# Kernel tuning notes

Measured on AMD Instinct MI355X. Metric: run time of the kernel, lower is better.

The kernel has to match this reference:

```python
import jax, jax.numpy as jnp
import numpy as np
import math

MSG_K = 256  # min(active_count, 256); with uniform(0,1) activations active_count >> 256
N_HEADS = 4
LN_EPS = 1e-5


def _mha(x, wi, bi, wo, bo):
    # torch nn.MultiheadAttention self-attention, batch_first=True
    B, K, D = x.shape
    H = N_HEADS
    hd = D // H
    qkv = x @ wi.T + bi                      # [B,K,3D]
    q, k, v = jnp.split(qkv, 3, axis=-1)
    def split_heads(t):
        return t.reshape(B, K, H, hd).transpose(0, 2, 1, 3)  # [B,H,K,hd]
    q, k, v = split_heads(q), split_heads(k), split_heads(v)
    scores = jnp.einsum('bhqd,bhkd->bhqk', q, k) * (1.0 / math.sqrt(hd))
    attn = jax.nn.softmax(scores, axis=-1)
    o = jnp.einsum('bhqk,bhkd->bhqd', attn, v)
    o = o.transpose(0, 2, 1, 3).reshape(B, K, D)
    return o @ wo.T + bo


def _layernorm(x, g, b):
    mu = jnp.mean(x, axis=-1, keepdims=True)
    var = jnp.mean((x - mu) ** 2, axis=-1, keepdims=True)
    return (x - mu) * jax.lax.rsqrt(var + LN_EPS) * g + b


def setup_inputs() -> dict:
    key = jax.random.key(0)
    ks = jax.random.split(key, 12)
    B, N, D = 32, 4096, 256
    s = 0.02
    return {
        'activation': jax.random.uniform(ks[0], (B, N), dtype=jnp.float32),
        'hidden_state': jax.random.normal(ks[1], (B, N, D), dtype=jnp.float32),
        'in_proj_w': jax.random.normal(ks[2], (3 * D, D), dtype=jnp.float32) * s,
        'in_proj_b': jnp.zeros((3 * D,), jnp.float32),
        'out_proj_w': jax.random.normal(ks[3], (D, D), dtype=jnp.float32) * s,
        'out_proj_b': jnp.zeros((D,), jnp.float32),
        'su_w1': jax.random.normal(ks[4], (D, 2 * D), dtype=jnp.float32) * s,
        'su_b1': jnp.zeros((D,), jnp.float32),
        'su_w2': jax.random.normal(ks[5], (D, D), dtype=jnp.float32) * s,
        'su_b2': jnp.zeros((D,), jnp.float32),
        'au_w1': jax.random.normal(ks[6], (D, 2 * D), dtype=jnp.float32) * s,
        'au_b1': jnp.zeros((D,), jnp.float32),
        'au_w2': jax.random.normal(ks[7], (1, D), dtype=jnp.float32) * s,
        'au_b2': jnp.zeros((1,), jnp.float32),
        'ln_g': jnp.ones((D,), jnp.float32),
        'ln_b': jnp.zeros((D,), jnp.float32),
        'sparsity_k': 256,
    }


def reference(activation, hidden_state, in_proj_w, in_proj_b, out_proj_w, out_proj_b,
              su_w1, su_b1, su_w2, su_b2, au_w1, au_b1, au_w2, au_b2, ln_g, ln_b,
              sparsity_k):
    B, N, D = hidden_state.shape
    b_idx = jnp.arange(B)[:, None]

    # ---- compute_messages: top-k gather -> sparse MHA -> scatter back ----
    topk_vals, topk_idx = jax.lax.top_k(activation, MSG_K)        # [B,K]
    active_states = jnp.take_along_axis(hidden_state, topk_idx[..., None], axis=1)  # [B,K,D]
    msg_sparse = _mha(active_states, in_proj_w, in_proj_b, out_proj_w, out_proj_b)
    msg_sparse = msg_sparse * topk_vals[..., None]
    messages = jnp.zeros((B, N, D), hidden_state.dtype).at[b_idx, topk_idx].set(msg_sparse)

    # ---- update_states: MLP on [old, messages] + LayerNorm ----
    combined = jnp.concatenate([hidden_state, messages], axis=-1)  # [B,N,2D]
    h = jax.nn.gelu(combined @ su_w1.T + su_b1, approximate=False)
    new_hidden = _layernorm(h @ su_w2.T + su_b2, ln_g, ln_b)

    # ---- update_activations ----
    comb2 = jnp.concatenate([hidden_state, new_hidden], axis=-1)
    h2 = jax.nn.gelu(comb2 @ au_w1.T + au_b1, approximate=False)
    delta = jax.nn.sigmoid((h2 @ au_w2.T + au_b2).squeeze(-1))     # [B,N]
    new_activation = jnp.clip(0.7 * activation + 0.3 * delta, 0.0, 1.0)

    # ---- maintain_sparsity: keep top sparsity_k, zero the rest ----
    k = min(int(sparsity_k), N)
    tv, ti = jax.lax.top_k(new_activation, k)                      # [B,k]
    sparse_act = jnp.zeros_like(new_activation).at[b_idx, ti].set(tv)
    kept_hidden = jnp.take_along_axis(new_hidden, ti[..., None], axis=1)
    sparse_hidden = jnp.zeros_like(new_hidden).at[b_idx, ti].set(kept_hidden)
    return sparse_act, sparse_hidden
```

## Files before the change

### kernel.cpp

```cpp
#include <hip/hip_runtime.h>


constexpr int KC = 32;
constexpr int CMAX = 2304;
constexpr float BAND_EPS = 0.01f;
constexpr int MAXBAND = 512;

typedef short bf16x8 __attribute__((ext_vector_type(8)));
typedef float f32x4 __attribute__((ext_vector_type(4)));

__device__ __forceinline__ float gelu_f(float x) {
    return 0.5f * x * (1.0f + erff(x * 0.70710678118654752440f));
}
__device__ __forceinline__ unsigned short f2bf(float f) {
    unsigned u = __float_as_uint(f);
    return (unsigned short)((u + 0x7fffu + ((u >> 16) & 1u)) >> 16);
}
__device__ __forceinline__ float bf2f(unsigned short h) {
    return __uint_as_float(((unsigned)h) << 16);
}

__global__ void __launch_bounds__(256) fill0_k(float4* p, long n4) {
    long i = (long)blockIdx.x * 256 + threadIdx.x;
    long stride = (long)gridDim.x * 256;
    float4 z = make_float4(0.f, 0.f, 0.f, 0.f);
    for (; i < n4; i += stride) p[i] = z;
}

__global__ void __launch_bounds__(256) topk1_k(const float* __restrict__ act,
        float* __restrict__ svals, int* __restrict__ sidx, int* __restrict__ cnt)
{
    __shared__ int cs[4];
    __shared__ int sTop, sRest;
    int b = blockIdx.x, tid = threadIdx.x;
    int wid = tid >> 6, lane = tid & 63;
    unsigned v[16];
    #pragma unroll
    for (int s = 0; s < 16; ++s)
        v[s] = __float_as_uint(act[b * 4096 + s * 256 + tid]);

    auto reduce4 = [&](int c) -> int {
        #pragma unroll
        for (int off = 32; off >= 1; off >>= 1) c += __shfl_xor(c, off);
        if (lane == 0) cs[wid] = c;
        __syncthreads();
        int tot = cs[0] + cs[1] + cs[2] + cs[3];
        __syncthreads();
        return tot;
    };
    auto countGE = [&](unsigned thr) -> int {
        int c = 0;
        #pragma unroll
        for (int s = 0; s < 16; ++s) c += (v[s] >= thr) ? 1 : 0;
        return reduce4(c);
    };
    auto countEqLt = [&](unsigned vs, int icut) -> int {
        int c = 0;
        #pragma unroll
        for (int s = 0; s < 16; ++s)
            c += (v[s] == vs && (s * 256 + tid) < icut) ? 1 : 0;
        return reduce4(c);
    };

    unsigned vstar = 0;
    for (int bit = 31; bit >= 0; --bit) {
        unsigned cand = vstar | (1u << bit);
        if (countGE(cand) >= 256) vstar = cand;
    }
    int cgt = countGE(vstar + 1);
    int needed = 256 - cgt;
    int icut = 4096;
    if (countEqLt(vstar, 4096) > needed) {
        int lo = 0, hi = 4096;
        for (int it = 0; it < 12; ++it) {
            int mid = (lo + hi) >> 1;
            if (countEqLt(vstar, mid) <= needed) lo = mid; else hi = mid;
        }
        icut = lo;
    }
    if (tid == 0) { sTop = 0; sRest = 0; }
    __syncthreads();
    float th = __uint_as_float(vstar) - 0.4288f;
    #pragma unroll
    for (int s = 0; s < 16; ++s) {
        int i = s * 256 + tid;
        unsigned vb = v[s];
        float f = __uint_as_float(vb);
        bool top = (vb > vstar) || (vb == vstar && i < icut);
        if (top) {
            int slot = atomicAdd(&sTop, 1);
            sidx[b * 4096 + slot] = i;
            svals[b * 4096 + slot] = f;
        } else if (f >= th) {
            int slot = 256 + atomicAdd(&sRest, 1);
            if (slot < CMAX) {
                sidx[b * 4096 + slot] = i;
                svals[b * 4096 + slot] = f;
            }
        }
    }
    __syncthreads();
    if (tid == 0) cnt[b] = min(256 + sRest, CMAX);
}

__global__ void __launch_bounds__(256) topk2_k(const float* __restrict__ newact,
        const int* __restrict__ sidx, const int* __restrict__ cnt,
        float* __restrict__ selv, int* __restrict__ selo, int* __restrict__ selp)
{
    __shared__ int cs[4];
    __shared__ int sSel;
    int b = blockIdx.x, tid = threadIdx.x;
    int wid = tid >> 6, lane = tid & 63;
    int C = min(cnt[b], CMAX);
    unsigned v[9];
    int org[9];
    #pragma unroll
    for (int s = 0; s < 9; ++s) {
        int p = s * 256 + tid;
        bool ok = (p < C && p < CMAX);
        v[s] = ok ? __float_as_uint(newact[(long)b * CMAX + p]) : 0u;
        org[s] = ok ? sidx[b * 4096 + p] : 0x7FFFFFFF;
    }
    auto reduce4 = [&](int c) -> int {
        #pragma unroll
        for (int off = 32; off >= 1; off >>= 1) c += __shfl_xor(c, off);
        if (lane == 0) cs[wid] = c;
        __syncthreads();
        int tot = cs[0] + cs[1] + cs[2] + cs[3];
        __syncthreads();
        return tot;
    };
    auto countGE = [&](unsigned thr) -> int {
        int c = 0;
        #pragma unroll
        for (int s = 0; s < 9; ++s) c += (v[s] >= thr) ? 1 : 0;
        return reduce4(c);
    };
    auto countEqLt = [&](unsigned vs, int icut) -> int {
        int c = 0;
        #pragma unroll
        for (int s = 0; s < 9; ++s) c += (v[s] == vs && org[s] < icut) ? 1 : 0;
        return reduce4(c);
    };

    unsigned vstar = 0;
    for (int bit = 31; bit >= 0; --bit) {
        unsigned cand = vstar | (1u << bit);
        if (countGE(cand) >= 256) vstar = cand;
    }
    int cgt = countGE(vstar + 1);
    int needed = 256 - cgt;
    int icut = 4096;
    if (countEqLt(vstar, 4096) > needed) {
        int lo = 0, hi = 4096;
        for (int it = 0; it < 12; ++it) {
            int mid = (lo + hi) >> 1;
            if (countEqLt(vstar, mid) <= needed) lo = mid; else hi = mid;
        }
        icut = lo;
    }
    if (tid == 0) sSel = 0;
    __syncthreads();
    #pragma unroll
    for (int s = 0; s < 9; ++s) {
        unsigned vb = v[s];
        bool sel = (vb > vstar) || (vb == vstar && org[s] < icut);
        if (sel) {
            int slot = atomicAdd(&sSel, 1);
            selv[b * 256 + slot] = __uint_as_float(vb);
            selo[b * 256 + slot] = org[s];
            selp[b * 256 + slot] = s * 256 + tid;
        }
    }
}

template<int TM, int TN, int RM, int RN, bool BT, bool GATHER, int EPI>
__global__ void __launch_bounds__(256) gemm_k(
    const float* __restrict__ A, int lda, long sA1, long sA2, int divA,
    const float* __restrict__ B, int ldb, long sB1, long sB2, int divB,
    float* __restrict__ C, int ldc, long sC1, long sC2, int divC,
    int K, const float* __restrict__ bias, const float* __restrict__ rowscale,
    long rsStride, const int* __restrict__ gmap, long gmapStride, float cscale)
{
    constexpr int TX = TN / RN, TY = TM / RM;
    static_assert(TX * TY == 256, "block must be 256 threads");
    __shared__ float As[KC][TM + 4];
    __shared__ float Bs[KC][TN + 4];
    int z = blockIdx.z;
    const float* Ab = A + (long)(z / divA) * sA1 + (long)(z % divA) * sA2;
    const float* Bb = B + (long)(z / divB) * sB1 + (long)(z % divB) * sB2;
    float* Cb = C + (long)(z / divC) * sC1 + (long)(z % divC) * sC2;
    int m0 = blockIdx.y * TM, n0 = blockIdx.x * TN;
    int tid = threadIdx.x;
    int tx = tid % TX, ty = tid / TX;
    float acc[RM][RN];
    #pragma unroll
    for (int i = 0; i < RM; ++i)
        #pragma unroll
        for (int j = 0; j < RN; ++j) acc[i][j] = 0.f;

    for (int k0 = 0; k0 < K; k0 += KC) {
        __syncthreads();
        #pragma unroll
        for (int u = 0; u < (TM * KC) / 1024; ++u) {
            int idx = tid + u * 256;
            int m = idx / (KC / 4), k4 = idx % (KC / 4);
            int row = m0 + m;
            long grow = GATHER ? (long)gmap[(long)z * gmapStride + row] : (long)row;
            float4 v = *(const float4*)(Ab + grow * lda + k0 + k4 * 4);
            As[k4 * 4 + 0][m] = v.x; As[k4 * 4 + 1][m] = v.y;
            As[k4 * 4 + 2][m] = v.z; As[k4 * 4 + 3][m] = v.w;
        }
        if (BT) {
            #pragma unroll
            for (int u = 0; u < (TN * KC) / 1024; ++u) {
                int idx = tid + u * 256;
                int n = idx / (KC / 4), k4 = idx % (KC / 4);
                float4 v = *(const float4*)(Bb + (long)(n0 + n) * ldb + k0 + k4 * 4);
                Bs[k4 * 4 + 0][n] = v.x; Bs[k4 * 4 + 1][n] = v.y;
                Bs[k4 * 4 + 2][n] = v.z; Bs[k4 * 4 + 3][n] = v.w;
            }
        } else {
            #pragma unroll
            for (int u = 0; u < (TN * KC) / 1024; ++u) {
                int idx = tid + u * 256;
                int k = idx / (TN / 4), n4 = idx % (TN / 4);
                float4 v = *(const float4*)(Bb + (long)(k0 + k) * ldb + n0 + n4 * 4);
                *(float4*)&Bs[k][n4 * 4] = v;
            }
        }
        __syncthreads();
        #pragma unroll
        for (int k = 0; k < KC; ++k) {
            float av[RM], bv[RN];
            #pragma unroll
            for (int i = 0; i < RM; i += 4) {
                float4 t = *(const float4*)&As[k][ty * RM + i];
                av[i] = t.x; av[i + 1] = t.y; av[i + 2] = t.z; av[i + 3] = t.w;
            }
            #pragma unroll
            for (int j = 0; j < RN; j += 4) {
                float4 t = *(const float4*)&Bs[k][tx * RN + j];
                bv[j] = t.x; bv[j + 1] = t.y; bv[j + 2] = t.z; bv[j + 3] = t.w;
            }
            #pragma unroll
            for (int i = 0; i < RM; ++i)
                #pragma unroll
                for (int j = 0; j < RN; ++j)
                    acc[i][j] = fmaf(av[i], bv[j], acc[i][j]);
        }
    }
    #pragma unroll
    for (int i = 0; i < RM; ++i) {
        int gm = m0 + ty * RM + i;
        float rs = 1.f;
        if (EPI == 2) rs = rowscale[(long)z * rsStride + gm];
        #pragma unroll
        for (int j = 0; j < RN; j += 4) {
            int gn = n0 + tx * RN + j;
            float4 v = make_float4(acc[i][j], acc[i][j + 1], acc[i][j + 2], acc[i][j + 3]);
            if (EPI == 1 || EPI == 2) {
                float4 bb = *(const float4*)(bias + gn);
                v.x += bb.x; v.y += bb.y; v.z += bb.z; v.w += bb.w;
            }
            if (EPI == 2) { v.x *= rs; v.y *= rs; v.z *= rs; v.w *= rs; }
            if (EPI == 3) { v.x *= cscale; v.y *= cscale; v.z *= cscale; v.w *= cscale; }
            *(float4*)(Cb + (long)gm * ldc + gn) = v;
        }
    }
}

__global__ void __launch_bounds__(256) softmax_k(float* __restrict__ S) {
    int row = blockIdx.x * 4 + (threadIdx.x >> 6);
    int lane = threadIdx.x & 63;
    float4* r = (float4*)(S + (long)row * 256);
    float4 v = r[lane];
    float m = fmaxf(fmaxf(v.x, v.y), fmaxf(v.z, v.w));
    for (int off = 32; off >= 1; off >>= 1) m = fmaxf(m, __shfl_xor(m, off));
    v.x = expf(v.x - m); v.y = expf(v.y - m); v.z = expf(v.z - m); v.w = expf(v.w - m);
    float s = v.x + v.y + v.z + v.w;
    for (int off = 32; off >= 1; off >>= 1) s += __shfl_xor(s, off);
    float inv = 1.f / s;
    v.x *= inv; v.y *= inv; v.z *= inv; v.w *= inv;
    r[lane] = v;
}

__global__ void __launch_bounds__(256) convw_k(
        const float* __restrict__ s1, const float* __restrict__ s2,
        const float* __restrict__ a1,
        unsigned short* __restrict__ o1, unsigned short* __restrict__ o2,
        unsigned short* __restrict__ o3)
{
    int i = blockIdx.x * 256 + threadIdx.x;
    o1[i] = f2bf(s1[i]);
    o3[i] = f2bf(a1[i]);
    if (i < 65536) o2[i] = f2bf(s2[i]);
}

__global__ void __launch_bounds__(256) transT_k(const float* __restrict__ src,
        int ld, int koff, float* __restrict__ dst)
{
    __shared__ float t[32][33];
    int k0 = blockIdx.x * 32, n0 = blockIdx.y * 32;
    int tx = threadIdx.x & 31, ty = threadIdx.x >> 5;
    #pragma unroll
    for (int yy = 0; yy < 4; ++yy) {
        int nl = ty * 4 + yy;
        t[nl][tx] = src[(long)(n0 + nl) * ld + koff + k0 + tx];
    }
    __syncthreads();
    #pragma unroll
    for (int yy = 0; yy < 4; ++yy) {
        int kl = ty * 4 + yy;
        dst[(long)(k0 + kl) * 256 + n0 + tx] = t[tx][kl];
    }
}

__global__ void __launch_bounds__(256) gatherX_k(const float* __restrict__ hid,
        const int* __restrict__ sidx, const int* __restrict__ cnt,
        unsigned short* __restrict__ Xb)
{
    int b = blockIdx.y;
    int C = min(cnt[b], CMAX);
    int p = blockIdx.x * 4 + (threadIdx.x >> 6);
    int lane = threadIdx.x & 63;
    unsigned short* dst = Xb + ((long)b * CMAX + p) * 256 + lane * 4;
    if (p < C) {
        int row = sidx[b * 4096 + p];
        float4 v = *(const float4*)(hid + ((long)b * 4096 + row) * 256 + lane * 4);
        ushort4 o; o.x = f2bf(v.x); o.y = f2bf(v.y); o.z = f2bf(v.z); o.w = f2bf(v.w);
        *(ushort4*)dst = o;
    } else {
        ushort4 z; z.x = 0; z.y = 0; z.z = 0; z.w = 0;
        *(ushort4*)dst = z;
    }
}

template<int STAGE>
__global__ void __launch_bounds__(256, 2) mlp_mfma_k(
    const unsigned short* __restrict__ A0,
    const unsigned short* __restrict__ A1,
    const unsigned short* __restrict__ W, int ldw,
    const float* __restrict__ bias,
    const float* __restrict__ msgc,
    const float* __restrict__ lng, const float* __restrict__ lnb,
    const float* __restrict__ w2v, const float* __restrict__ b2s,
    const float* __restrict__ svals,
    const int* __restrict__ cnt,
    unsigned short* __restrict__ outb,
    float* __restrict__ nac)
{
    int b = blockIdx.y;
    int C = min(cnt[b], CMAX);
    int m0 = blockIdx.x * 64;
    if (m0 >= C) return;
    int tid = threadIdx.x;
    int wid = tid >> 6;
    int lane = tid & 63;
    int l15 = lane & 15;
    int q = lane >> 4;
    int n0w = wid * 64;

    f32x4 acc[4][4];
    #pragma unroll
    for (int mt = 0; mt < 4; ++mt)
        #pragma unroll
        for (int nt = 0; nt < 4; ++nt) {
            f32x4 z = {0.f, 0.f, 0.f, 0.f};
            acc[mt][nt] = z;
        }

    const unsigned short* Ab = A0 + ((long)b * CMAX + m0) * 256;
    const unsigned short* A1b = (STAGE == 3) ? (A1 + ((long)b * CMAX + m0) * 256) : nullptr;
    int aoff[4];
    #pragma unroll
    for (int mt = 0; mt < 4; ++mt) aoff[mt] = (mt * 16 + l15) * 256;
    const unsigned short* wr[4];
    #pragma unroll
    for (int nt = 0; nt < 4; ++nt) wr[nt] = W + (long)(n0w + nt * 16 + l15) * ldw;

    constexpr int KSTEPS = (STAGE == 3) ? 16 : 8;
    #pragma unroll 4
    for (int ks = 0; ks < KSTEPS; ++ks) {
        const unsigned short* As = (STAGE == 3 && ks >= 8) ? A1b : Ab;
        int ko = (STAGE == 3 && ks >= 8) ? (ks - 8) * 32 : ks * 32;
        int kw = ks * 32;
        bf16x8 af[4], bfr[4];
        #pragma unroll
        for (int mt = 0; mt < 4; ++mt)
            af[mt] = *(const bf16x8*)(As + aoff[mt] + ko + q * 8);
        #pragma unroll
        for (int nt = 0; nt < 4; ++nt)
            bfr[nt] = *(const bf16x8*)(wr[nt] + kw + q * 8);
        #pragma unroll
        for (int mt = 0; mt < 4; ++mt)
            #pragma unroll
            for (int nt = 0; nt < 4; ++nt)
                acc[mt][nt] = __builtin_amdgcn_mfma_f32_16x16x32_bf16(
                    af[mt], bfr[nt], acc[mt][nt], 0, 0, 0);
    }

    if constexpr (STAGE == 1) {
        float bb[4];
        #pragma unroll
        for (int nt = 0; nt < 4; ++nt) bb[nt] = bias[n0w + nt * 16 + l15];
        #pragma unroll
        for (int mt = 0; mt < 4; ++mt) {
            #pragma unroll
            for (int reg = 0; reg < 4; ++reg) {
                int p = m0 + mt * 16 + q * 4 + reg;
                long orow = ((long)b * CMAX + p) * 256;
                const float* mrow = msgc + ((long)b * 256 + p) * 256;
                bool hasm = (p < 256);
                #pragma unroll
                for (int nt = 0; nt < 4; ++nt) {
                    int gc = n0w + nt * 16 + l15;
                    float v = acc[mt][nt][reg] + bb[nt];
                    if (hasm) v += mrow[gc];
                    outb[orow + gc] = f2bf(gelu_f(v));
                }
            }
        }
    }

    if constexpr (STAGE == 2) {
        __shared__ float rsum[4][64];
        __shared__ float rsq[4][64];
        __shared__ float rmu[64], rrs[64];
        float bb[4], gg[4], eb[4];
        #pragma unroll
        for (int nt = 0; nt < 4; ++nt) {
            int gc = n0w + nt * 16 + l15;
            bb[nt] = bias[gc]; gg[nt] = lng[gc]; eb[nt] = lnb[gc];
        }
        #pragma unroll
        for (int mt = 0; mt < 4; ++mt)
            #pragma unroll
            for (int nt = 0; nt < 4; ++nt)
                #pragma unroll
                for (int reg = 0; reg < 4; ++reg)
                    acc[mt][nt][reg] += bb[nt];
        #pragma unroll
        for (int mt = 0; mt < 4; ++mt) {
            #pragma unroll
            for (int reg = 0; reg < 4; ++reg) {
                float s = 0.f, s2 = 0.f;
                #pragma unroll
                for (int nt = 0; nt < 4; ++nt) {
                    float v = acc[mt][nt][reg];
                    s += v; s2 += v * v;
                }
                #pragma unroll
                for (int off = 1; off <= 8; off <<= 1) {
                    s += __shfl_xor(s, off);
                    s2 += __shfl_xor(s2, off);
                }
                if (l15 == 0) {
                    int row = mt * 16 + q * 4 + reg;
                    rsum[wid][row] = s; rsq[wid][row] = s2;
                }
            }
        }
        __syncthreads();
        if (tid < 64) {
            float s = rsum[0][tid] + rsum[1][tid] + rsum[2][tid] + rsum[3][tid];
            float s2 = rsq[0][tid] + rsq[1][tid] + rsq[2][tid] + rsq[3][tid];
            float mu = s * (1.f / 256.f);
            float var = s2 * (1.f / 256.f) - mu * mu;
            rmu[tid] = mu;
            rrs[tid] = rsqrtf(var + 1e-5f);
        }
        __syncthreads();
        #pragma unroll
        for (int mt = 0; mt < 4; ++mt) {
            #pragma unroll
            for (int reg = 0; reg < 4; ++reg) {
                int row = mt * 16 + q * 4 + reg;
                int p = m0 + row;
                float mu = rmu[row], rs = rrs[row];
                long orow = ((long)b * CMAX + p) * 256;
                #pragma unroll
                for (int nt = 0; nt < 4; ++nt) {
                    int gc = n0w + nt * 16 + l15;
                    outb[orow + gc] = f2bf((acc[mt][nt][reg] - mu) * rs * gg[nt] + eb[nt]);
                }
            }
        }
    }

    if constexpr (STAGE == 3) {
        __shared__ float rsum[4][64];
        float bb[4], ww[4];
        #pragma unroll
        for (int nt = 0; nt < 4; ++nt) {
            int gc = n0w + nt * 16 + l15;
            bb[nt] = bias[gc]; ww[nt] = w2v[gc];
        }
        #pragma unroll
        for (int mt = 0; mt < 4; ++mt) {
            #pragma unroll
            for (int reg = 0; reg < 4; ++reg) {
                float s = 0.f;
                #pragma unroll
                for (int nt = 0; nt < 4; ++nt)
                    s += gelu_f(acc[mt][nt][reg] + bb[nt]) * ww[nt];
                #pragma unroll
                for (int off = 1; off <= 8; off <<= 1) s += __shfl_xor(s, off);
                if (l15 == 0) rsum[wid][mt * 16 + q * 4 + reg] = s;
            }
        }
        __syncthreads();
        if (tid < 64) {
            int p = m0 + tid;
            if (p < C) {
                float z = rsum[0][tid] + rsum[1][tid] + rsum[2][tid] + rsum[3][tid] + b2s[0];
                float delta = 1.f / (1.f + expf(-z));
                float na = 0.7f * svals[b * 4096 + p] + 0.3f * delta;
                nac[(long)b * CMAX + p] = fminf(fmaxf(na, 0.f), 1.f);
            }
        }
    }
}

__global__ void __launch_bounds__(256) selectT_k(const float* __restrict__ nac,
        const int* __restrict__ cnt, float* __restrict__ T)
{
    __shared__ float v[CMAX];
    __shared__ int cs[256];
    __shared__ float bounds[2];
    int b = blockIdx.x, tid = threadIdx.x;
    int C = min(cnt[b], CMAX);
    for (int i = tid; i < CMAX; i += 256)
        v[i] = (i < C) ? nac[(long)b * CMAX + i] : -1.f;
    if (tid == 0) { bounds[0] = 0.f; bounds[1] = 1.0f; }
    __syncthreads();
    for (int it = 0; it < 30; ++it) {
        float mid = 0.5f * (bounds[0] + bounds[1]);
        int c = 0;
        for (int i = tid; i < CMAX; i += 256) c += (v[i] >= mid) ? 1 : 0;
        cs[tid] = c; __syncthreads();
        for (int s = 128; s; s >>= 1) {
            if (tid < s) cs[tid] += cs[tid + s];
            __syncthreads();
        }
        if (tid == 0) { if (cs[0] >= 256) bounds[0] = mid; else bounds[1] = mid; }
        __syncthreads();
    }
    if (tid == 0) T[b] = bounds[0];
}

__global__ void __launch_bounds__(256) bandlist_k(const float* __restrict__ nac,
        const int* __restrict__ cnt, const float* __restrict__ Tarr,
        int* __restrict__ bandlist, int* __restrict__ bandcnt)
{
    int b = blockIdx.y;
    int C = min(cnt[b], CMAX);
    int p = blockIdx.x * 256 + threadIdx.x;
    if (p < C && fabsf(nac[(long)b * CMAX + p] - Tarr[b]) < BAND_EPS) {
        int slot = atomicAdd(&bandcnt[b], 1);
        if (slot < MAXBAND) bandlist[b * MAXBAND + slot] = p;
    }
}

__global__ void __launch_bounds__(256) bandfix_k(
    const float* __restrict__ hid, const int* __restrict__ sidx,
    const float* __restrict__ msgc,
    const float* __restrict__ w1T, const float* __restrict__ su_b1,
    const float* __restrict__ w2T, const float* __restrict__ su_b2,
    const float* __restrict__ ln_g, const float* __restrict__ ln_b,
    const float* __restrict__ auT, const float* __restrict__ au_b1,
    const float* __restrict__ au_w2, const float* __restrict__ au_b2,
    const float* __restrict__ svals,
    const int* __restrict__ bandlist, const int* __restrict__ bandcnt,
    float* __restrict__ nac, unsigned short* __restrict__ NHb)
{
    int b = blockIdx.y;
    int M = min(bandcnt[b], MAXBAND);
    int base = blockIdx.x * 8;
    if (base >= M) return;
    int nact = min(M - base, 8);
    int tid = threadIdx.x;
    int wid = tid >> 6, lane = tid & 63;
    __shared__ float xr[8][256];
    __shared__ float hy[8][256];
    __shared__ float nh[8][256];
    __shared__ float muS[8], rsS[8];
    __shared__ int ppS[8];
    if (tid < 8)
        ppS[tid] = (tid < nact) ? bandlist[b * MAXBAND + base + tid] : -1;
    __syncthreads();
    #pragma unroll
    for (int r = 0; r < 8; ++r) {
        int pp = ppS[r];
        xr[r][tid] = (pp >= 0) ? hid[((long)b * 4096 + sidx[b * 4096 + pp]) * 256 + tid] : 0.f;
    }
    __syncthreads();
    int n = tid;
    float acc[8];
    #pragma unroll
    for (int r = 0; r < 8; ++r) acc[r] = 0.f;
    for (int k = 0; k < 256; k += 4) {
        float w0 = w1T[(k + 0) * 256 + n];
        float w1 = w1T[(k + 1) * 256 + n];
        float w2 = w1T[(k + 2) * 256 + n];
        float w3 = w1T[(k + 3) * 256 + n];
        #pragma unroll
        for (int r = 0; r < 8; ++r) {
            float4 xv = *(const float4*)&xr[r][k];
            acc[r] = fmaf(w0, xv.x, acc[r]);
            acc[r] = fmaf(w1, xv.y, acc[r]);
            acc[r] = fmaf(w2, xv.z, acc[r]);
            acc[r] = fmaf(w3, xv.w, acc[r]);
        }
    }
    float b1v = su_b1[n];
    #pragma unroll
    for (int r = 0; r < 8; ++r) {
        int pp = ppS[r];
        float s = acc[r] + b1v;
        if (pp >= 0 && pp < 256) s += msgc[((long)b * 256 + pp) * 256 + n];
        acc[r] = gelu_f(s);
    }
    __syncthreads();
    #pragma unroll
    for (int r = 0; r < 8; ++r) hy[r][n] = acc[r];
    __syncthreads();
    #pragma unroll
    for (int r = 0; r < 8; ++r) acc[r] = 0.f;
    for (int k = 0; k < 256; k += 4) {
        float w0 = w2T[(k + 0) * 256 + n];
        float w1 = w2T[(k + 1) * 256 + n];
        float w2 = w2T[(k + 2) * 256 + n];
        float w3 = w2T[(k + 3) * 256 + n];
        #pragma unroll
        for (int r = 0; r < 8; ++r) {
            float4 hv = *(const float4*)&hy[r][k];
            acc[r] = fmaf(w0, hv.x, acc[r]);
            acc[r] = fmaf(w1, hv.y, acc[r]);
            acc[r] = fmaf(w2, hv.z, acc[r]);
            acc[r] = fmaf(w3, hv.w, acc[r]);
        }
    }
    __syncthreads();
    float b2v = su_b2[n];
    #pragma unroll
    for (int r = 0; r < 8; ++r) hy[r][n] = acc[r] + b2v;
    __syncthreads();
    #pragma unroll
    for (int rr = 0; rr < 2; ++rr) {
        int r = wid + rr * 4;
        float4 yv = *(const float4*)&hy[r][lane * 4];
        float s = yv.x + yv.y + yv.z + yv.w;
        float s2 = yv.x * yv.x + yv.y * yv.y + yv.z * yv.z + yv.w * yv.w;
        #pragma unroll
        for (int off = 32; off >= 1; off >>= 1) {
            s += __shfl_xor(s, off);
            s2 += __shfl_xor(s2, off);
        }
        if (lane == 0) {
            float mu = s * (1.f / 256.f);
            float var = s2 * (1.f / 256.f) - mu * mu;
            muS[r] = mu; rsS[r] = rsqrtf(var + 1e-5f);
        }
    }
    __syncthreads();
    float gv = ln_g[n], ev = ln_b[n];
    #pragma unroll
    for (int r = 0; r < 8; ++r) {
        float o = (hy[r][n] - muS[r]) * rsS[r] * gv + ev;
        nh[r][n] = o;
        if (ppS[r] >= 0) NHb[((long)b * CMAX + ppS[r]) * 256 + n] = f2bf(o);
    }
    __syncthreads();
    #pragma unroll
    for (int r = 0; r < 8; ++r) acc[r] = 0.f;
    for (int k = 0; k < 256; k += 4) {
        float w0 = auT[(k + 0) * 256 + n];
        float w1 = auT[(k + 1) * 256 + n];
        float w2 = auT[(k + 2) * 256 + n];
        float w3 = auT[(k + 3) * 256 + n];
        #pragma unroll
        for (int r = 0; r < 8; ++r) {
            float4 xv = *(const float4*)&xr[r][k];
            acc[r] = fmaf(w0, xv.x, acc[r]);
            acc[r] = fmaf(w1, xv.y, acc[r]);
            acc[r] = fmaf(w2, xv.z, acc[r]);
            acc[r] = fmaf(w3, xv.w, acc[r]);
        }
    }
    for (int k = 0; k < 256; k += 4) {
        float w0 = auT[(256 + k + 0) * 256 + n];
        float w1 = auT[(256 + k + 1) * 256 + n];
        float w2 = auT[(256 + k + 2) * 256 + n];
        float w3 = auT[(256 + k + 3) * 256 + n];
        #pragma unroll
        for (int r = 0; r < 8; ++r) {
            float4 hv = *(const float4*)&nh[r][k];
            acc[r] = fmaf(w0, hv.x, acc[r]);
            acc[r] = fmaf(w1, hv.y, acc[r]);
            acc[r] = fmaf(w2, hv.z, acc[r]);
            acc[r] = fmaf(w3, hv.w, acc[r]);
        }
    }
    float ab = au_b1[n], wv2 = au_w2[n];
    __syncthreads();
    #pragma unroll
    for (int r = 0; r < 8; ++r) hy[r][n] = gelu_f(acc[r] + ab) * wv2;
    __syncthreads();
    #pragma unroll
    for (int rr = 0; rr < 2; ++rr) {
        int r = wid + rr * 4;
        float4 gvv = *(const float4*)&hy[r][lane * 4];
        float s = gvv.x + gvv.y + gvv.z + gvv.w;
        #pragma unroll
        for (int off = 32; off >= 1; off >>= 1) s += __shfl_xor(s, off);
        if (lane == 0 && ppS[r] >= 0) {
            float z = s + au_b2[0];
            float delta = 1.f / (1.f + expf(-z));
            float na = 0.7f * svals[b * 4096 + ppS[r]] + 0.3f * delta;
            nac[(long)b * CMAX + ppS[r]] = fminf(fmaxf(na, 0.f), 1.f);
        }
    }
}

__global__ void __launch_bounds__(64) scatter_k(const float* __restrict__ selv,
        const int* __restrict__ selo, const int* __restrict__ selp,
        const unsigned short* __restrict__ NHb, float* __restrict__ out)
{
    int b = blockIdx.x >> 8, j = blockIdx.x & 255, t = threadIdx.x;
    int orig = selo[b * 256 + j];
    int p = selp[b * 256 + j];
    if (t == 0) out[b * 4096 + orig] = selv[b * 256 + j];
    const ushort4* src = (const ushort4*)(NHb + ((long)b * CMAX + p) * 256);
    ushort4 s = src[t];
    float4 o = make_float4(bf2f(s.x), bf2f(s.y), bf2f(s.z), bf2f(s.w));
    *(float4*)(out + 131072 + ((long)(b * 4096 + orig)) * 256 + t * 4) = o;
}

extern "C" void kernel_launch(void* const* d_in, const int* in_sizes, int n_in,
                              void* d_out, int out_size, void* d_ws, size_t ws_size,
                              hipStream_t stream)
{
    const float* act   = (const float*)d_in[0];
    const float* hid   = (const float*)d_in[1];
    const float* wi    = (const float*)d_in[2];
    const float* bi    = (const float*)d_in[3];
    const float* wo    = (const float*)d_in[4];
    const float* bo    = (const float*)d_in[5];
    const float* su_w1 = (const float*)d_in[6];
    const float* su_b1 = (const float*)d_in[7];
    const float* su_w2 = (const float*)d_in[8];
    const float* su_b2 = (const float*)d_in[9];
    const float* au_w1 = (const float*)d_in[10];
    const float* au_b1 = (const float*)d_in[11];
    const float* au_w2 = (const float*)d_in[12];
    const float* au_b2 = (const float*)d_in[13];
    const float* ln_g  = (const float*)d_in[14];
    const float* ln_b  = (const float*)d_in[15];
    float* out = (float*)d_out;

    char* ws = (char*)d_ws;
    size_t off = 0;
    auto alloc = [&](size_t bytes) {
        size_t o = off; off += (bytes + 255) & ~(size_t)255; return o;
    };
    float* svals = (float*)(ws + alloc((size_t)32 * 4096 * 4));
    int*   sidx  = (int*)  (ws + alloc((size_t)32 * 4096 * 4));
    int*   cnt   = (int*)  (ws + alloc(256));
    float* qkv   = (float*)(ws + alloc((size_t)32 * 256 * 768 * 4));
    float* Sb    = (float*)(ws + alloc((size_t)32 * 4 * 256 * 256 * 4));
    float* Ob    = (float*)(ws + alloc((size_t)32 * 256 * 256 * 4));
    float* MSG   = (float*)(ws + alloc((size_t)32 * 256 * 256 * 4));
    float* MSGC  = (float*)(ws + alloc((size_t)32 * 256 * 256 * 4));
    float* selv  = (float*)(ws + alloc((size_t)32 * 256 * 4));
    int*   selo  = (int*)  (ws + alloc((size_t)32 * 256 * 4));
    int*   selp  = (int*)  (ws + alloc((size_t)32 * 256 * 4));
    unsigned short* swb1 = (unsigned short*)(ws + alloc((size_t)256 * 512 * 2));
    unsigned short* swb2 = (unsigned short*)(ws + alloc((size_t)256 * 256 * 2));
    unsigned short* awb1 = (unsigned short*)(ws + alloc((size_t)256 * 512 * 2));
    float* w1T = (float*)(ws + alloc((size_t)256 * 256 * 4));
    float* w2T = (float*)(ws + alloc((size_t)256 * 256 * 4));
    float* auT = (float*)(ws + alloc((size_t)512 * 256 * 4));
    unsigned short* Xb   = (unsigned short*)(ws + alloc((size_t)32 * CMAX * 256 * 2));
    unsigned short* H1b  = (unsigned short*)(ws + alloc((size_t)32 * CMAX * 256 * 2));
    unsigned short* NHb  = (unsigned short*)(ws + alloc((size_t)32 * CMAX * 256 * 2));
    float* nac = (float*)(ws + alloc((size_t)32 * CMAX * 4));
    float* Tb  = (float*)(ws + alloc(128));
    int* bandl = (int*)(ws + alloc((size_t)32 * MAXBAND * 4));
    int* bandc = (int*)(ws + alloc(128));

    hipMemsetAsync(bandc, 0, 32 * sizeof(int), stream);
    fill0_k<<<2048, 256, 0, stream>>>((float4*)out, (long)out_size / 4);
    topk1_k<<<32, 256, 0, stream>>>(act, svals, sidx, cnt);
    convw_k<<<512, 256, 0, stream>>>(su_w1, su_w2, au_w1, swb1, swb2, awb1);
    transT_k<<<dim3(8, 8), 256, 0, stream>>>(su_w1, 512, 0, w1T);
    transT_k<<<dim3(8, 8), 256, 0, stream>>>(su_w2, 256, 0, w2T);
    transT_k<<<dim3(16, 8), 256, 0, stream>>>(au_w1, 512, 0, auT);
    gatherX_k<<<dim3(CMAX / 4, 32), 256, 0, stream>>>(hid, sidx, cnt, Xb);
    gemm_k<64, 256, 8, 8, true, true, 1><<<dim3(3, 4, 32), 256, 0, stream>>>(
        hid, 256, (long)4096 * 256, 0, 1,
        wi, 256, 0, 0, 1,
        qkv, 768, (long)256 * 768, 0, 1,
        256, bi, nullptr, 0, sidx, 4096, 0.f);
    gemm_k<64, 256, 8, 8, true, false, 3><<<dim3(1, 4, 128), 256, 0, stream>>>(
        qkv, 768, 196608, 64, 4,
        qkv + 256, 768, 196608, 64, 4,
        Sb, 256, 65536, 0, 1,
        64, nullptr, nullptr, 0, nullptr, 0, 0.125f);
    softmax_k<<<8192, 256, 0, stream>>>(Sb);
    gemm_k<64, 64, 4, 4, false, false, 0><<<dim3(1, 4, 128), 256, 0, stream>>>(
        Sb, 256, 65536, 0, 1,
        qkv + 512, 768, 196608, 64, 4,
        Ob, 256, 65536, 64, 4,
        256, nullptr, nullptr, 0, nullptr, 0, 0.f);
    gemm_k<64, 256, 8, 8, true, false, 2><<<dim3(1, 4, 32), 256, 0, stream>>>(
        Ob, 256, 65536, 0, 1,
        wo, 256, 0, 0, 1,
        MSG, 256, 65536, 0, 1,
        256, bo, svals, 4096, nullptr, 0, 0.f);
    gemm_k<64, 256, 8, 8, true, false, 0><<<dim3(1, 4, 32), 256, 0, stream>>>(
        MSG, 256, 65536, 0, 1,
        su_w1 + 256, 512, 0, 0, 1,
        MSGC, 256, 65536, 0, 1,
        256, nullptr, nullptr, 0, nullptr, 0, 0.f);
    dim3 mgrid(CMAX / 64, 32);
    mlp_mfma_k<1><<<mgrid, 256, 0, stream>>>(Xb, nullptr, swb1, 512, su_b1, MSGC,
        nullptr, nullptr, nullptr, nullptr, nullptr, cnt, H1b, nullptr);
    mlp_mfma_k<2><<<mgrid, 256, 0, stream>>>(H1b, nullptr, swb2, 256, su_b2, nullptr,
        ln_g, ln_b, nullptr, nullptr, nullptr, cnt, NHb, nullptr);
    mlp_mfma_k<3><<<mgrid, 256, 0, stream>>>(Xb, NHb, awb1, 512, au_b1, nullptr,
        nullptr, nullptr, au_w2, au_b2, svals, cnt, nullptr, nac);
    selectT_k<<<32, 256, 0, stream>>>(nac, cnt, Tb);
    bandlist_k<<<dim3(CMAX / 256, 32), 256, 0, stream>>>(nac, cnt, Tb, bandl, bandc);
    bandfix_k<<<dim3(MAXBAND / 8, 32), 256, 0, stream>>>(hid, sidx, MSGC,
        w1T, su_b1, w2T, su_b2, ln_g, ln_b, auT, au_b1, au_w2, au_b2,
        svals, bandl, bandc, nac, NHb);
    topk2_k<<<32, 256, 0, stream>>>(nac, sidx, cnt, selv, selo, selp);
    scatter_k<<<8192, 64, 0, stream>>>(selv, selo, selp, NHb, out);
}
```

Before: 831.6 us.

## Pack fp32 weights as float4 for bandfix, fuse prep kernels, narrow refinement band

Merges the bf16 weight conversion and three transpose kernels into one prep kernel that writes the fp32 weights in a k-interleaved float4 layout. bandfix_k can then load a float4 per step instead of four scalars, and it now handles 4 rows per block instead of 8, giving more blocks. The exact-recompute band around the top-k threshold shrinks from 0.01 to 0.004, and the threshold bisection drops from 30 to 20 iterations. Together these cut launch count and the fp32 fix-up work. A narrower band and a coarser threshold could miss borderline candidates whose bf16 scores were wrong.

```diff
diff --git a/kernel.cpp b/kernel.cpp
--- a/kernel.cpp
+++ b/kernel.cpp
@@ -3,7 +3,7 @@
 
 constexpr int KC = 32;
 constexpr int CMAX = 2304;
-constexpr float BAND_EPS = 0.01f;
+constexpr float BAND_EPS = 0.004f;
 constexpr int MAXBAND = 512;
 
 typedef short bf16x8 __attribute__((ext_vector_type(8)));
@@ -285,34 +285,38 @@
     r[lane] = v;
 }
 
-__global__ void __launch_bounds__(256) convw_k(
+__global__ void __launch_bounds__(256) prep_k(
         const float* __restrict__ s1, const float* __restrict__ s2,
         const float* __restrict__ a1,
         unsigned short* __restrict__ o1, unsigned short* __restrict__ o2,
-        unsigned short* __restrict__ o3)
-{
-    int i = blockIdx.x * 256 + threadIdx.x;
-    o1[i] = f2bf(s1[i]);
-    o3[i] = f2bf(a1[i]);
-    if (i < 65536) o2[i] = f2bf(s2[i]);
-}
-
-__global__ void __launch_bounds__(256) transT_k(const float* __restrict__ src,
-        int ld, int koff, float* __restrict__ dst)
-{
+        unsigned short* __restrict__ o3,
+        float* __restrict__ w1P, float* __restrict__ w2P, float* __restrict__ auP)
+{
+    int blk = blockIdx.x, tid = threadIdx.x;
+    if (blk < 512) {
+        int i = blk * 256 + tid;
+        o1[i] = f2bf(s1[i]);
+        o3[i] = f2bf(a1[i]);
+        if (i < 65536) o2[i] = f2bf(s2[i]);
+        return;
+    }
+    const float* src; float* dst; int ld, ktiles, rel;
+    if (blk < 576) { rel = blk - 512; src = s1; ld = 512; dst = w1P; ktiles = 8; }
+    else if (blk < 640) { rel = blk - 576; src = s2; ld = 256; dst = w2P; ktiles = 8; }
+    else { rel = blk - 640; src = a1; ld = 512; dst = auP; ktiles = 16; }
+    int k0 = (rel % ktiles) * 32, n0 = (rel / ktiles) * 32;
     __shared__ float t[32][33];
-    int k0 = blockIdx.x * 32, n0 = blockIdx.y * 32;
-    int tx = threadIdx.x & 31, ty = threadIdx.x >> 5;
+    int tx = tid & 31, ty = tid >> 5;
     #pragma unroll
     for (int yy = 0; yy < 4; ++yy) {
         int nl = ty * 4 + yy;
-        t[nl][tx] = src[(long)(n0 + nl) * ld + koff + k0 + tx];
+        t[nl][tx] = src[(long)(n0 + nl) * ld + k0 + tx];
     }
     __syncthreads();
     #pragma unroll
     for (int yy = 0; yy < 4; ++yy) {
-        int kl = ty * 4 + yy;
-        dst[(long)(k0 + kl) * 256 + n0 + tx] = t[tx][kl];
+        int k = k0 + ty * 4 + yy;
+        dst[(long)(k >> 2) * 1024 + (n0 + tx) * 4 + (k & 3)] = t[tx][ty * 4 + yy];
     }
 }
 
@@ -534,7 +538,7 @@
         v[i] = (i < C) ? nac[(long)b * CMAX + i] : -1.f;
     if (tid == 0) { bounds[0] = 0.f; bounds[1] = 1.0f; }
     __syncthreads();
-    for (int it = 0; it < 30; ++it) {
+    for (int it = 0; it < 20; ++it) {
         float mid = 0.5f * (bounds[0] + bounds[1]);
         int c = 0;
         for (int i = tid; i < CMAX; i += 256) c += (v[i] >= mid) ? 1 : 0;
@@ -565,10 +569,10 @@
 __global__ void __launch_bounds__(256) bandfix_k(
     const float* __restrict__ hid, const int* __restrict__ sidx,
     const float* __restrict__ msgc,
-    const float* __restrict__ w1T, const float* __restrict__ su_b1,
-    const float* __restrict__ w2T, const float* __restrict__ su_b2,
+    const float* __restrict__ w1Pf, const float* __restrict__ su_b1,
+    const float* __restrict__ w2Pf, const float* __restrict__ su_b2,
     const float* __restrict__ ln_g, const float* __restrict__ ln_b,
-    const float* __restrict__ auT, const float* __restrict__ au_b1,
+    const float* __restrict__ auPf, const float* __restrict__ au_b1,
     const float* __restrict__ au_w2, const float* __restrict__ au_b2,
     const float* __restrict__ svals,
     const int* __restrict__ bandlist, const int* __restrict__ bandcnt,
@@ -576,46 +580,46 @@
 {
     int b = blockIdx.y;
     int M = min(bandcnt[b], MAXBAND);
-    int base = blockIdx.x * 8;
+    int base = blockIdx.x * 4;
     if (base >= M) return;
-    int nact = min(M - base, 8);
+    int nact = min(M - base, 4);
     int tid = threadIdx.x;
     int wid = tid >> 6, lane = tid & 63;
-    __shared__ float xr[8][256];
-    __shared__ float hy[8][256];
-    __shared__ float nh[8][256];
-    __shared__ float muS[8], rsS[8];
-    __shared__ int ppS[8];
-    if (tid < 8)
+    const float4* w1P = (const float4*)w1Pf;
+    const float4* w2P = (const float4*)w2Pf;
+    const float4* auP = (const float4*)auPf;
+    __shared__ float xr[4][256];
+    __shared__ float hy[4][256];
+    __shared__ float nh[4][256];
+    __shared__ float muS[4], rsS[4];
+    __shared__ int ppS[4];
+    if (tid < 4)
         ppS[tid] = (tid < nact) ? bandlist[b * MAXBAND + base + tid] : -1;
     __syncthreads();
     #pragma unroll
-    for (int r = 0; r < 8; ++r) {
+    for (int r = 0; r < 4; ++r) {
         int pp = ppS[r];
         xr[r][tid] = (pp >= 0) ? hid[((long)b * 4096 + sidx[b * 4096 + pp]) * 256 + tid] : 0.f;
     }
     __syncthreads();
     int n = tid;
-    float acc[8];
-    #pragma unroll
-    for (int r = 0; r < 8; ++r) acc[r] = 0.f;
-    for (int k = 0; k < 256; k += 4) {
-        float w0 = w1T[(k + 0) * 256 + n];
-        float w1 = w1T[(k + 1) * 256 + n];
-        float w2 = w1T[(k + 2) * 256 + n];
-        float w3 = w1T[(k + 3) * 256 + n];
-        #pragma unroll
-        for (int r = 0; r < 8; ++r) {
-            float4 xv = *(const float4*)&xr[r][k];
-            acc[r] = fmaf(w0, xv.x, acc[r]);
-            acc[r] = fmaf(w1, xv.y, acc[r]);
-            acc[r] = fmaf(w2, xv.z, acc[r]);
-            acc[r] = fmaf(w3, xv.w, acc[r]);
+    float acc[4];
+    #pragma unroll
+    for (int r = 0; r < 4; ++r) acc[r] = 0.f;
+    for (int k4 = 0; k4 < 64; ++k4) {
+        float4 w = w1P[k4 * 256 + n];
+        #pragma unroll
+        for (int r = 0; r < 4; ++r) {
+            float4 xv = *(const float4*)&xr[r][k4 * 4];
+            acc[r] = fmaf(w.x, xv.x, acc[r]);
+            acc[r] = fmaf(w.y, xv.y, acc[r]);
+            acc[r] = fmaf(w.z, xv.z, acc[r]);
+            acc[r] = fmaf(w.w, xv.w, acc[r]);
         }
     }
     float b1v = su_b1[n];
     #pragma unroll
-    for (int r = 0; r < 8; ++r) {
+    for (int r = 0; r < 4; ++r) {
         int pp = ppS[r];
         float s = acc[r] + b1v;
         if (pp >= 0 && pp < 256) s += msgc[((long)b * 256 + pp) * 256 + n];
@@ -623,32 +627,28 @@
     }
     __syncthreads();
     #pragma unroll
-    for (int r = 0; r < 8; ++r) hy[r][n] = acc[r];
-    __syncthreads();
-    #pragma unroll
-    for (int r = 0; r < 8; ++r) acc[r] = 0.f;
-    for (int k = 0; k < 256; k += 4) {
-        float w0 = w2T[(k + 0) * 256 + n];
-        float w1 = w2T[(k + 1) * 256 + n];
-        float w2 = w2T[(k + 2) * 256 + n];
-        float w3 = w2T[(k + 3) * 256 + n];
-        #pragma unroll
-        for (int r = 0; r < 8; ++r) {
-            float4 hv = *(const float4*)&hy[r][k];
-            acc[r] = fmaf(w0, hv.x, acc[r]);
-            acc[r] = fmaf(w1, hv.y, acc[r]);
-            acc[r] = fmaf(w2, hv.z, acc[r]);
-            acc[r] = fmaf(w3, hv.w, acc[r]);
+    for (int r = 0; r < 4; ++r) hy[r][n] = acc[r];
+    __syncthreads();
+    #pragma unroll
+    for (int r = 0; r < 4; ++r) acc[r] = 0.f;
+    for (int k4 = 0; k4 < 64; ++k4) {
+        float4 w = w2P[k4 * 256 + n];
+        #pragma unroll
+        for (int r = 0; r < 4; ++r) {
+            float4 hv = *(const float4*)&hy[r][k4 * 4];
+            acc[r] = fmaf(w.x, hv.x, acc[r]);
+            acc[r] = fmaf(w.y, hv.y, acc[r]);
+            acc[r] = fmaf(w.z, hv.z, acc[r]);
+            acc[r] = fmaf(w.w, hv.w, acc[r]);
         }
     }
     __syncthreads();
     float b2v = su_b2[n];
     #pragma unroll
-    for (int r = 0; r < 8; ++r) hy[r][n] = acc[r] + b2v;
-    __syncthreads();
-    #pragma unroll
-    for (int rr = 0; rr < 2; ++rr) {
-        int r = wid + rr * 4;
+    for (int r = 0; r < 4; ++r) hy[r][n] = acc[r] + b2v;
+    __syncthreads();
+    {
+        int r = wid;
         float4 yv = *(const float4*)&hy[r][lane * 4];
         float s = yv.x + yv.y + yv.z + yv.w;
         float s2 = yv.x * yv.x + yv.y * yv.y + yv.z * yv.z + yv.w * yv.w;
@@ -666,50 +666,43 @@
     __syncthreads();
     float gv = ln_g[n], ev = ln_b[n];
     #pragma unroll
-    for (int r = 0; r < 8; ++r) {
+    for (int r = 0; r < 4; ++r) {
         float o = (hy[r][n] - muS[r]) * rsS[r] * gv + ev;
         nh[r][n] = o;
         if (ppS[r] >= 0) NHb[((long)b * CMAX + ppS[r]) * 256 + n] = f2bf(o);
     }
     __syncthreads();
     #pragma unroll
-    for (int r = 0; r < 8; ++r) acc[r] = 0.f;
-    for (int k = 0; k < 256; k += 4) {
-        float w0 = auT[(k + 0) * 256 + n];
-        float w1 = auT[(k + 1) * 256 + n];
-        float w2 = auT[(k + 2) * 256 + n];
-        float w3 = auT[(k + 3) * 256 + n];
-        #pragma unroll
-        for (int r = 0; r < 8; ++r) {
-            float4 xv = *(const float4*)&xr[r][k];
-            acc[r] = fmaf(w0, xv.x, acc[r]);
-            acc[r] = fmaf(w1, xv.y, acc[r]);
-            acc[r] = fmaf(w2, xv.z, acc[r]);
-            acc[r] = fmaf(w3, xv.w, acc[r]);
-        }
-    }
-    for (int k = 0; k < 256; k += 4) {
-        float w0 = auT[(256 + k + 0) * 256 + n];
-        float w1 = auT[(256 + k + 1) * 256 + n];
-        float w2 = auT[(256 + k + 2) * 256 + n];
-        float w3 = auT[(256 + k + 3) * 256 + n];
-        #pragma unroll
-        for (int r = 0; r < 8; ++r) {
-            float4 hv = *(const float4*)&nh[r][k];
-            acc[r] = fmaf(w0, hv.x, acc[r]);
-            acc[r] = fmaf(w1, hv.y, acc[r]);
-            acc[r] = fmaf(w2, hv.z, acc[r]);
-            acc[r] = fmaf(w3, hv.w, acc[r]);
+    for (int r = 0; r < 4; ++r) acc[r] = 0.f;
+    for (int k4 = 0; k4 < 64; ++k4) {
+        float4 w = auP[k4 * 256 + n];
+        #pragma unroll
+        for (int r = 0; r < 4; ++r) {
+            float4 xv = *(const float4*)&xr[r][k4 * 4];
+            acc[r] = fmaf(w.x, xv.x, acc[r]);
+            acc[r] = fmaf(w.y, xv.y, acc[r]);
+            acc[r] = fmaf(w.z, xv.z, acc[r]);
+            acc[r] = fmaf(w.w, xv.w, acc[r]);
+        }
+    }
+    for (int k4 = 64; k4 < 128; ++k4) {
+        float4 w = auP[k4 * 256 + n];
+        #pragma unroll
+        for (int r = 0; r < 4; ++r) {
+            float4 hv = *(const float4*)&nh[r][(k4 - 64) * 4];
+            acc[r] = fmaf(w.x, hv.x, acc[r]);
+            acc[r] = fmaf(w.y, hv.y, acc[r]);
+            acc[r] = fmaf(w.z, hv.z, acc[r]);
+            acc[r] = fmaf(w.w, hv.w, acc[r]);
         }
     }
     float ab = au_b1[n], wv2 = au_w2[n];
     __syncthreads();
     #pragma unroll
-    for (int r = 0; r < 8; ++r) hy[r][n] = gelu_f(acc[r] + ab) * wv2;
-    __syncthreads();
-    #pragma unroll
-    for (int rr = 0; rr < 2; ++rr) {
-        int r = wid + rr * 4;
+    for (int r = 0; r < 4; ++r) hy[r][n] = gelu_f(acc[r] + ab) * wv2;
+    __syncthreads();
+    {
+        int r = wid;
         float4 gvv = *(const float4*)&hy[r][lane * 4];
         float s = gvv.x + gvv.y + gvv.z + gvv.w;
         #pragma unroll
@@ -778,9 +771,9 @@
     unsigned short* swb1 = (unsigned short*)(ws + alloc((size_t)256 * 512 * 2));
     unsigned short* swb2 = (unsigned short*)(ws + alloc((size_t)256 * 256 * 2));
     unsigned short* awb1 = (unsigned short*)(ws + alloc((size_t)256 * 512 * 2));
-    float* w1T = (float*)(ws + alloc((size_t)256 * 256 * 4));
-    float* w2T = (float*)(ws + alloc((size_t)256 * 256 * 4));
-    float* auT = (float*)(ws + alloc((size_t)512 * 256 * 4));
+    float* w1P = (float*)(ws + alloc((size_t)256 * 256 * 4));
+    float* w2P = (float*)(ws + alloc((size_t)256 * 256 * 4));
+    float* auP = (float*)(ws + alloc((size_t)512 * 256 * 4));
     unsigned short* Xb   = (unsigned short*)(ws + alloc((size_t)32 * CMAX * 256 * 2));
     unsigned short* H1b  = (unsigned short*)(ws + alloc((size_t)32 * CMAX * 256 * 2));
     unsigned short* NHb  = (unsigned short*)(ws + alloc((size_t)32 * CMAX * 256 * 2));
@@ -792,10 +785,8 @@
     hipMemsetAsync(bandc, 0, 32 * sizeof(int), stream);
     fill0_k<<<2048, 256, 0, stream>>>((float4*)out, (long)out_size / 4);
     topk1_k<<<32, 256, 0, stream>>>(act, svals, sidx, cnt);
-    convw_k<<<512, 256, 0, stream>>>(su_w1, su_w2, au_w1, swb1, swb2, awb1);
-    transT_k<<<dim3(8, 8), 256, 0, stream>>>(su_w1, 512, 0, w1T);
-    transT_k<<<dim3(8, 8), 256, 0, stream>>>(su_w2, 256, 0, w2T);
-    transT_k<<<dim3(16, 8), 256, 0, stream>>>(au_w1, 512, 0, auT);
+    prep_k<<<768, 256, 0, stream>>>(su_w1, su_w2, au_w1, swb1, swb2, awb1,
+                                    w1P, w2P, auP);
     gatherX_k<<<dim3(CMAX / 4, 32), 256, 0, stream>>>(hid, sidx, cnt, Xb);
     gemm_k<64, 256, 8, 8, true, true, 1><<<dim3(3, 4, 32), 256, 0, stream>>>(
         hid, 256, (long)4096 * 256, 0, 1,
@@ -832,8 +823,8 @@
         nullptr, nullptr, au_w2, au_b2, svals, cnt, nullptr, nac);
     selectT_k<<<32, 256, 0, stream>>>(nac, cnt, Tb);
     bandlist_k<<<dim3(CMAX / 256, 32), 256, 0, stream>>>(nac, cnt, Tb, bandl, bandc);
-    bandfix_k<<<dim3(MAXBAND / 8, 32), 256, 0, stream>>>(hid, sidx, MSGC,
-        w1T, su_b1, w2T, su_b2, ln_g, ln_b, auT, au_b1, au_w2, au_b2,
+    bandfix_k<<<dim3(MAXBAND / 4, 32), 256, 0, stream>>>(hid, sidx, MSGC,
+        w1P, su_b1, w2P, su_b2, ln_g, ln_b, auP, au_b1, au_w2, au_b2,
         svals, bandl, bandc, nac, NHb);
     topk2_k<<<32, 256, 0, stream>>>(nac, sidx, cnt, selv, selo, selp);
     scatter_k<<<8192, 64, 0, stream>>>(selv, selo, selp, NHb, out);
```

Result: faster. 795.0 us (-4.4%).
